# Optimization experiments

Measured on AMD Instinct MI355X. Metric: run time of the kernel, lower is better.

The kernel has to match this reference:

```python
import jax, jax.numpy as jnp
import numpy as np

N_NODES = 100000
N_EDGES = 1600000
D_IN = 128
D_OUT = 128
LN_EPS = 1e-5
MEAN_EPS = 1e-8


def setup_inputs() -> dict:
    key = jax.random.key(0)
    ks = jax.random.split(key, 8)
    x = jax.random.normal(ks[0], (N_NODES, D_IN), dtype=jnp.float32)
    edge_index = jax.random.randint(ks[1], (2, N_EDGES), 0, N_NODES, dtype=jnp.int64)
    s = 1.0 / np.sqrt(D_IN)
    W_agg = jax.random.uniform(ks[2], (D_OUT, D_IN), jnp.float32, -s, s)
    b_agg = jax.random.uniform(ks[3], (D_OUT,), jnp.float32, -s, s)
    W_self = jax.random.uniform(ks[4], (D_OUT, D_IN), jnp.float32, -s, s)
    b_self = jax.random.uniform(ks[5], (D_OUT,), jnp.float32, -s, s)
    gamma = jnp.ones((D_OUT,), jnp.float32)
    beta = jnp.zeros((D_OUT,), jnp.float32)
    return {"x": x, "edge_index": edge_index, "W_agg": W_agg, "b_agg": b_agg,
            "W_self": W_self, "b_self": b_self, "gamma": gamma, "beta": beta}


def reference(x, edge_index, W_agg, b_agg, W_self, b_self, gamma, beta):
    row, col = edge_index[0], edge_index[1]
    num_nodes = x.shape[0]
    # self path: Linear(in, out)
    self_out = x @ W_self.T + b_self                              # [N, D_OUT]
    # mean aggregation: fused gather + segment-sum (no index_add buffer passes)
    neighbor_sum = jax.ops.segment_sum(x[col], row, num_segments=num_nodes)   # [N, D_IN]
    ones = jnp.ones((col.shape[0], 1), dtype=x.dtype)
    neighbor_count = jax.ops.segment_sum(ones, row, num_segments=num_nodes)   # [N, 1]
    neighbor_mean = neighbor_sum / (neighbor_count + MEAN_EPS)
    agg_out = neighbor_mean @ W_agg.T + b_agg                     # [N, D_OUT]
    # relu -> LayerNorm (dropout is identity at eval)
    h = jax.nn.relu(self_out + agg_out)
    mu = jnp.mean(h, axis=-1, keepdims=True)
    var = jnp.mean(jnp.square(h - mu), axis=-1, keepdims=True)
    return (h - mu) * jax.lax.rsqrt(var + LN_EPS) * gamma + beta
```

## Files before the change

### kernel.cpp

```cpp
#include <hip/hip_runtime.h>

#define N_NODES 100000
#define N_EDGES 1600000
#define D 128
#define RPB 64
#define NBUCKET 1563
#define NBLK 196
#define EPB 8192
#define AGG_CAP 2048
#define XCB 3125
#define SCAN_PAD 1792

constexpr float LN_EPS   = 1e-5f;
constexpr float MEAN_EPS = 1e-8f;

typedef __attribute__((ext_vector_type(8))) short bf16x8;
typedef __attribute__((ext_vector_type(4))) float f32x4;

__device__ inline float bf2f(unsigned short h) {
  union { unsigned u; float f; } v; v.u = (unsigned)h << 16; return v.f;
}
__device__ inline float bflo(unsigned p) {
  union { unsigned u; float f; } v; v.u = p << 16; return v.f;
}
__device__ inline float bfhi(unsigned p) {
  union { unsigned u; float f; } v; v.u = p & 0xFFFF0000u; return v.f;
}
__device__ inline unsigned short f2bf(float f) {
  union { float f; unsigned u; } v; v.f = f;
  return (unsigned short)((v.u + 0x7FFFu + ((v.u >> 16) & 1u)) >> 16);
}

__global__ __launch_bounds__(256) void prep_sort(
    const float* __restrict__ x, const int* __restrict__ ei,
    const float* __restrict__ Wself, const float* __restrict__ Wagg,
    const float* __restrict__ bself, const float* __restrict__ bagg,
    unsigned short* __restrict__ xb, unsigned short* __restrict__ wcat,
    float* __restrict__ bsum, unsigned* __restrict__ ent_sorted,
    int* __restrict__ chunkoff) {
  __shared__ int ent_s[EPB];
  __shared__ int cnt_s[SCAN_PAD];
  __shared__ int off_s[SCAN_PAD];
  __shared__ int sb[256];
  const int bid = blockIdx.x;
  const int t = threadIdx.x;

  if (bid < NBLK) {
    const int ebase = bid * EPB;
    const int nch = min(EPB, N_EDGES - ebase);
    const int base4 = bid * (EPB / 4);
    const int end4 = base4 + (nch >> 2);

    for (int i = t; i < SCAN_PAD; i += 256) cnt_s[i] = 0;
    __syncthreads();

#pragma unroll
    for (int k = 0; k < EPB / 1024; ++k) {
      int i4 = base4 + k * 256 + t;
      if (i4 < end4) {
        int4 r = ((const int4*)ei)[i4];
        atomicAdd(&cnt_s[r.x >> 6], 1);
        atomicAdd(&cnt_s[r.y >> 6], 1);
        atomicAdd(&cnt_s[r.z >> 6], 1);
        atomicAdd(&cnt_s[r.w >> 6], 1);
      }
    }
    __syncthreads();

    int psum = 0;
#pragma unroll
    for (int i = 0; i < 7; ++i) psum += cnt_s[t * 7 + i];
    sb[t] = psum;
    __syncthreads();
    for (int off = 1; off < 256; off <<= 1) {
      int u = (t >= off) ? sb[t - off] : 0;
      __syncthreads();
      sb[t] += u;
      __syncthreads();
    }
    int run = sb[t] - psum;
#pragma unroll
    for (int i = 0; i < 7; ++i) {
      off_s[t * 7 + i] = run;
      run += cnt_s[t * 7 + i];
    }
    __syncthreads();

    for (int b = t; b < NBUCKET; b += 256)
      chunkoff[b * NBLK + bid] = off_s[b] | (cnt_s[b] << 14);
    __syncthreads();

#pragma unroll
    for (int k = 0; k < EPB / 1024; ++k) {
      int i4 = base4 + k * 256 + t;
      if (i4 < end4) {
        int4 r = ((const int4*)ei)[i4];
        int4 c = ((const int4*)(ei + N_EDGES))[i4];
        int p0 = atomicAdd(&off_s[r.x >> 6], 1);
        ent_s[p0] = ((r.x & 63) << 17) | c.x;
        int p1 = atomicAdd(&off_s[r.y >> 6], 1);
        ent_s[p1] = ((r.y & 63) << 17) | c.y;
        int p2 = atomicAdd(&off_s[r.z >> 6], 1);
        ent_s[p2] = ((r.z & 63) << 17) | c.z;
        int p3 = atomicAdd(&off_s[r.w >> 6], 1);
        ent_s[p3] = ((r.w & 63) << 17) | c.w;
      }
    }
    __syncthreads();

    for (int i = t; i < nch; i += 256)
      ent_sorted[ebase + i] = (unsigned)ent_s[i];
  } else if (bid < NBLK + XCB) {
    const int base = (bid - NBLK) * 1024;
#pragma unroll
    for (int k = 0; k < 4; ++k) {
      int i4 = base + k * 256 + t;
      float4 v = ((const float4*)x)[i4];
      ushort4 o;
      o.x = f2bf(v.x); o.y = f2bf(v.y); o.z = f2bf(v.z); o.w = f2bf(v.w);
      ((ushort4*)xb)[i4] = o;
    }
  } else {
    const int blk = bid - NBLK - XCB;
#pragma unroll
    for (int k = 0; k < 8; ++k) {
      int idx = blk * 2048 + k * 256 + t;
      int o = idx >> 8, kc = idx & 255;
      float v = (kc < 128) ? Wself[o * 128 + kc] : Wagg[o * 128 + (kc - 128)];
      wcat[o * 256 + kc] = f2bf(v);
    }
    if (blk == 0 && t < 128) bsum[t] = bself[t] + bagg[t];
  }
}

__global__ __launch_bounds__(256) void aggregate(
    const unsigned short* __restrict__ xb, const unsigned* __restrict__ ent_sorted,
    const int* __restrict__ chunkoff, float* out) {
  __shared__ int ent_s[AGG_CAP];
  __shared__ int col_s[AGG_CAP];
  __shared__ int sb[256];
  __shared__ int cnt_s[RPB];
  __shared__ int off_s[RPB];
  __shared__ int cur_s[RPB];

  const int b = blockIdx.x;
  const int t = threadIdx.x;

  int beg = 0, len = 0;
  if (t < NBLK) {
    int pk = chunkoff[b * NBLK + t];
    beg = pk & 16383;
    len = pk >> 14;
  }
  sb[t] = len;
  __syncthreads();
  for (int off = 1; off < 256; off <<= 1) {
    int u = (t >= off) ? sb[t - off] : 0;
    __syncthreads();
    sb[t] += u;
    __syncthreads();
  }
  int n = sb[255]; if (n > AGG_CAP) n = AGG_CAP;
  int dst = sb[t] - len;
  if (t < NBLK) {
    const unsigned* src = ent_sorted + t * EPB + beg;
    for (int i = 0; i < len; ++i)
      if (dst + i < AGG_CAP) ent_s[dst + i] = (int)src[i];
  }
  __syncthreads();

  if (t < RPB) cnt_s[t] = 0;
  __syncthreads();
  for (int i = t; i < n; i += 256) atomicAdd(&cnt_s[ent_s[i] >> 17], 1);
  __syncthreads();
  if (t < RPB) off_s[t] = cnt_s[t];
  __syncthreads();
  for (int off = 1; off < RPB; off <<= 1) {
    int u = 0;
    if (t < RPB && t >= off) u = off_s[t - off];
    __syncthreads();
    if (t < RPB) off_s[t] += u;
    __syncthreads();
  }
  int excl = 0;
  if (t < RPB) excl = off_s[t] - cnt_s[t];
  __syncthreads();
  if (t < RPB) { off_s[t] = excl; cur_s[t] = excl; }
  __syncthreads();
  for (int i = t; i < n; i += 256) {
    int e = ent_s[i];
    int pos = atomicAdd(&cur_s[e >> 17], 1);
    col_s[pos] = e & 0x1FFFF;
  }
  __syncthreads();

  const int w = t >> 6, lane = t & 63;
  const int nodebase = b << 6;
  for (int lrow = w; lrow < RPB; lrow += 4) {
    int node = nodebase + lrow;
    if (node >= N_NODES) break;
    int rbeg = off_s[lrow];
    int deg = cnt_s[lrow];
    float a0 = 0.f, a1 = 0.f;
    int j = 0;
    for (; j + 8 <= deg; j += 8) {
      unsigned p[8];
#pragma unroll
      for (int u = 0; u < 8; ++u) {
        int col = col_s[rbeg + j + u];
        p[u] = *(const unsigned*)(xb + (size_t)col * D + lane * 2);
      }
#pragma unroll
      for (int u = 0; u < 8; ++u) { a0 += bflo(p[u]); a1 += bfhi(p[u]); }
    }
    if (j + 4 <= deg) {
      unsigned p[4];
#pragma unroll
      for (int u = 0; u < 4; ++u) {
        int col = col_s[rbeg + j + u];
        p[u] = *(const unsigned*)(xb + (size_t)col * D + lane * 2);
      }
#pragma unroll
      for (int u = 0; u < 4; ++u) { a0 += bflo(p[u]); a1 += bfhi(p[u]); }
      j += 4;
    }
    for (; j < deg; ++j) {
      int col = col_s[rbeg + j];
      unsigned p = *(const unsigned*)(xb + (size_t)col * D + lane * 2);
      a0 += bflo(p); a1 += bfhi(p);
    }
    float inv = 1.0f / ((float)deg + MEAN_EPS);
    unsigned o = (unsigned)f2bf(a0 * inv) | ((unsigned)f2bf(a1 * inv) << 16);
    ((unsigned*)(out + (size_t)node * D))[lane] = o;
  }
}

__global__ __launch_bounds__(512, 4) void gemm_mfma_ln(
    const unsigned short* __restrict__ xb, const float* out_mean,
    const unsigned short* __restrict__ wcat, const float* __restrict__ bsum,
    const float* __restrict__ gamma, const float* __restrict__ beta,
    float* out) {
  __shared__ unsigned short Bs[128 * 264];
  __shared__ float bias_s[128];

  const int t = threadIdx.x;
  const int w = t >> 6, lane = t & 63;
  const int q = lane >> 4, s = lane & 15;
  const int base = blockIdx.x * 128;

  if (t < 128) bias_s[t] = bsum[t];

#pragma unroll
  for (int r = 0; r < 8; ++r) {
    int f = r * 512 + t;
    int row = f >> 5, c = f & 31;
    uint4 v = *(const uint4*)(wcat + row * 256 + c * 8);
    *(uint4*)(Bs + row * 264 + c * 8) = v;
  }

  const int arow = base + w * 16 + s;
  const int asafe = (arow < N_NODES) ? arow : 0;
  const unsigned short* xrow = xb + (size_t)asafe * 128;
  const unsigned short* mrow = (const unsigned short*)(out_mean + (size_t)asafe * 128);
  bf16x8 a[8];
#pragma unroll
  for (int kk = 0; kk < 4; ++kk)
    a[kk] = *(const bf16x8*)(xrow + kk * 32 + q * 8);
#pragma unroll
  for (int kk = 0; kk < 4; ++kk)
    a[4 + kk] = *(const bf16x8*)(mrow + kk * 32 + q * 8);

  __syncthreads();

  f32x4 acc[8];
#pragma unroll
  for (int j = 0; j < 8; ++j) acc[j] = (f32x4)(0.0f);

#pragma unroll
  for (int kk = 0; kk < 8; ++kk) {
    const int ko = kk * 32 + q * 8;
#pragma unroll
    for (int j = 0; j < 8; ++j) {
      bf16x8 bv = *(const bf16x8*)(Bs + (j * 16 + s) * 264 + ko);
      acc[j] = __builtin_amdgcn_mfma_f32_16x16x32_bf16(a[kk], bv, acc[j], 0, 0, 0);
    }
  }

#pragma unroll
  for (int j = 0; j < 8; ++j) {
    float bb = bias_s[j * 16 + s];
#pragma unroll
    for (int r = 0; r < 4; ++r)
      acc[j][r] = fmaxf(acc[j][r] + bb, 0.0f);
  }

  float g[8], be[8];
#pragma unroll
  for (int j = 0; j < 8; ++j) {
    g[j]  = gamma[j * 16 + s];
    be[j] = beta[j * 16 + s];
  }

#pragma unroll
  for (int r = 0; r < 4; ++r) {
    float s1 = 0.f, s2 = 0.f;
#pragma unroll
    for (int j = 0; j < 8; ++j) {
      float h = acc[j][r];
      s1 += h; s2 += h * h;
    }
#pragma unroll
    for (int m = 1; m < 16; m <<= 1) {
      s1 += __shfl_xor(s1, m, 64);
      s2 += __shfl_xor(s2, m, 64);
    }
    int node = base + w * 16 + q * 4 + r;
    if (node < N_NODES) {
      float mu = s1 * (1.0f / 128.0f);
      float var = s2 * (1.0f / 128.0f) - mu * mu;
      float rstd = rsqrtf(var + LN_EPS);
      float* orow = out + (size_t)node * 128;
#pragma unroll
      for (int j = 0; j < 8; ++j)
        orow[j * 16 + s] = (acc[j][r] - mu) * rstd * g[j] + be[j];
    }
  }
}

extern "C" void kernel_launch(void* const* d_in, const int* in_sizes, int n_in,
                              void* d_out, int out_size, void* d_ws, size_t ws_size,
                              hipStream_t stream) {
  const float* x     = (const float*)d_in[0];
  const int*   ei    = (const int*)d_in[1];
  const float* Wagg  = (const float*)d_in[2];
  const float* bagg  = (const float*)d_in[3];
  const float* Wself = (const float*)d_in[4];
  const float* bself = (const float*)d_in[5];
  const float* gamma = (const float*)d_in[6];
  const float* beta  = (const float*)d_in[7];
  float* out = (float*)d_out;

  unsigned short* xb   = (unsigned short*)d_ws;
  unsigned short* wcat = xb + (size_t)N_NODES * D;
  float* bsum      = (float*)(wcat + 128 * 256);
  unsigned* ent_sorted = (unsigned*)(bsum + 128);
  int* chunkoff    = (int*)(ent_sorted + (size_t)NBLK * EPB);

  prep_sort<<<NBLK + XCB + 16, 256, 0, stream>>>(
      x, ei, Wself, Wagg, bself, bagg, xb, wcat, bsum, ent_sorted, chunkoff);

  aggregate<<<NBUCKET, 256, 0, stream>>>(xb, ent_sorted, chunkoff, out);

  gemm_mfma_ln<<<(N_NODES + 127) / 128, 512, 0, stream>>>(
      xb, out, wcat, bsum, gamma, beta, out);
}
```

Baseline: 215.4 us.

## Split aggregation into row-sort pass and feature-sliced gather kernel

The fused aggregate kernel is split in two. A row_sort kernel does the per-bucket counting sort and writes the sorted column lists and per-row offset/degree info to workspace. An agg_slice kernel then launches eight blocks per bucket, each gathering one 16-feature slice with 8-lane groups, so 32 rows are processed concurrently per block for more memory-level parallelism. The cost is an extra launch, an extra global round trip for the sorted indices, and 32-byte gather segments instead of full 256-byte rows. AGG_CAP is also cut to 1280, which risks overflow for buckets with unusually many edges.

```diff
diff --git a/kernel.cpp b/kernel.cpp
--- a/kernel.cpp
+++ b/kernel.cpp
@@ -7,9 +7,10 @@
 #define NBUCKET 1563
 #define NBLK 196
 #define EPB 8192
-#define AGG_CAP 2048
+#define AGG_CAP 1280
 #define XCB 3125
 #define SCAN_PAD 1792
+#define NSLICE 8
 
 constexpr float LN_EPS   = 1e-5f;
 constexpr float MEAN_EPS = 1e-8f;
@@ -17,9 +18,6 @@
 typedef __attribute__((ext_vector_type(8))) short bf16x8;
 typedef __attribute__((ext_vector_type(4))) float f32x4;
 
-__device__ inline float bf2f(unsigned short h) {
-  union { unsigned u; float f; } v; v.u = (unsigned)h << 16; return v.f;
-}
 __device__ inline float bflo(unsigned p) {
   union { unsigned u; float f; } v; v.u = p << 16; return v.f;
 }
@@ -133,9 +131,9 @@
   }
 }
 
-__global__ __launch_bounds__(256) void aggregate(
-    const unsigned short* __restrict__ xb, const unsigned* __restrict__ ent_sorted,
-    const int* __restrict__ chunkoff, float* out) {
+__global__ __launch_bounds__(256) void row_sort(
+    const unsigned* __restrict__ ent_sorted, const int* __restrict__ chunkoff,
+    unsigned* __restrict__ col_sorted, unsigned* __restrict__ rowinfo) {
   __shared__ int ent_s[AGG_CAP];
   __shared__ int col_s[AGG_CAP];
   __shared__ int sb[256];
@@ -194,21 +192,47 @@
   }
   __syncthreads();
 
-  const int w = t >> 6, lane = t & 63;
-  const int nodebase = b << 6;
-  for (int lrow = w; lrow < RPB; lrow += 4) {
-    int node = nodebase + lrow;
-    if (node >= N_NODES) break;
-    int rbeg = off_s[lrow];
-    int deg = cnt_s[lrow];
+  for (int i = t; i < n; i += 256)
+    __builtin_nontemporal_store((unsigned)col_s[i],
+                                col_sorted + (size_t)b * AGG_CAP + i);
+  if (t < RPB)
+    __builtin_nontemporal_store((unsigned)off_s[t] | ((unsigned)cnt_s[t] << 16),
+                                rowinfo + b * RPB + t);
+}
+
+__global__ __launch_bounds__(256) void agg_slice(
+    const unsigned short* __restrict__ xb, const unsigned* __restrict__ col_sorted,
+    const unsigned* __restrict__ rowinfo, float* __restrict__ out) {
+  __shared__ unsigned cols_s[AGG_CAP];
+  __shared__ unsigned ri_s[RPB];
+
+  const int bid = blockIdx.x;
+  const int g = bid & 7;
+  const int b = bid >> 3;
+  const int t = threadIdx.x;
+
+  if (t < RPB) ri_s[t] = __builtin_nontemporal_load(rowinfo + b * RPB + t);
+  __syncthreads();
+  const int n = (int)(ri_s[RPB - 1] & 0xFFFFu) + (int)(ri_s[RPB - 1] >> 16);
+  for (int i = t; i < n; i += 256)
+    cols_s[i] = __builtin_nontemporal_load(col_sorted + (size_t)b * AGG_CAP + i);
+  __syncthreads();
+
+  const int grp = t >> 3, gl = t & 7;
+  const unsigned short* xg = xb + g * 16 + gl * 2;
+
+  for (int rr = grp; rr < RPB; rr += 32) {
+    const unsigned ri = ri_s[rr];
+    const int rbeg = (int)(ri & 0xFFFFu);
+    const int deg = (int)(ri >> 16);
     float a0 = 0.f, a1 = 0.f;
     int j = 0;
     for (; j + 8 <= deg; j += 8) {
       unsigned p[8];
 #pragma unroll
       for (int u = 0; u < 8; ++u) {
-        int col = col_s[rbeg + j + u];
-        p[u] = *(const unsigned*)(xb + (size_t)col * D + lane * 2);
+        unsigned col = cols_s[rbeg + j + u];
+        p[u] = *(const unsigned*)(xg + (size_t)col * 128);
       }
 #pragma unroll
       for (int u = 0; u < 8; ++u) { a0 += bflo(p[u]); a1 += bfhi(p[u]); }
@@ -217,21 +241,24 @@
       unsigned p[4];
 #pragma unroll
       for (int u = 0; u < 4; ++u) {
-        int col = col_s[rbeg + j + u];
-        p[u] = *(const unsigned*)(xb + (size_t)col * D + lane * 2);
+        unsigned col = cols_s[rbeg + j + u];
+        p[u] = *(const unsigned*)(xg + (size_t)col * 128);
       }
 #pragma unroll
       for (int u = 0; u < 4; ++u) { a0 += bflo(p[u]); a1 += bfhi(p[u]); }
       j += 4;
     }
     for (; j < deg; ++j) {
-      int col = col_s[rbeg + j];
-      unsigned p = *(const unsigned*)(xb + (size_t)col * D + lane * 2);
+      unsigned col = cols_s[rbeg + j];
+      unsigned p = *(const unsigned*)(xg + (size_t)col * 128);
       a0 += bflo(p); a1 += bfhi(p);
     }
-    float inv = 1.0f / ((float)deg + MEAN_EPS);
-    unsigned o = (unsigned)f2bf(a0 * inv) | ((unsigned)f2bf(a1 * inv) << 16);
-    ((unsigned*)(out + (size_t)node * D))[lane] = o;
+    const int node = (b << 6) + rr;
+    if (node < N_NODES) {
+      float inv = 1.0f / ((float)deg + MEAN_EPS);
+      unsigned o = (unsigned)f2bf(a0 * inv) | ((unsigned)f2bf(a1 * inv) << 16);
+      __builtin_nontemporal_store(o, (unsigned*)(out + (size_t)node * D) + g * 8 + gl);
+    }
   }
 }
 
@@ -345,11 +372,15 @@
   float* bsum      = (float*)(wcat + 128 * 256);
   unsigned* ent_sorted = (unsigned*)(bsum + 128);
   int* chunkoff    = (int*)(ent_sorted + (size_t)NBLK * EPB);
+  unsigned* col_sorted = (unsigned*)(chunkoff + (size_t)NBUCKET * NBLK);
+  unsigned* rowinfo    = col_sorted + (size_t)NBUCKET * AGG_CAP;
 
   prep_sort<<<NBLK + XCB + 16, 256, 0, stream>>>(
       x, ei, Wself, Wagg, bself, bagg, xb, wcat, bsum, ent_sorted, chunkoff);
 
-  aggregate<<<NBUCKET, 256, 0, stream>>>(xb, ent_sorted, chunkoff, out);
+  row_sort<<<NBUCKET, 256, 0, stream>>>(ent_sorted, chunkoff, col_sorted, rowinfo);
+
+  agg_slice<<<NBUCKET * NSLICE, 256, 0, stream>>>(xb, col_sorted, rowinfo, out);
 
   gemm_mfma_ln<<<(N_NODES + 127) / 128, 512, 0, stream>>>(
       xb, out, wcat, bsum, gamma, beta, out);
```

After: 333.8 us. +55.0%, slower.
